# Kernel tuning notes

Hardware: AMD Instinct MI355X
Metric: run time of the kernel (lower is better)

## Reference

```python
import jax, jax.numpy as jnp
import numpy as np

NUM_HEADS = 8
LN_EPS = 1e-3  # keras LayerNormalization default epsilon


def _layer_norm(z, gamma, beta):
    m = jnp.mean(z, axis=-1, keepdims=True)
    v = jnp.mean(jnp.square(z - m), axis=-1, keepdims=True)
    return (z - m) * jax.lax.rsqrt(v + LN_EPS) * gamma + beta


def _swish(z):
    return z * jax.nn.sigmoid(z)


def setup_inputs() -> dict:
    key = jax.random.key(0)
    ks = jax.random.split(key, 9)
    B, T, F, U = 64, 256, 512, 1024
    he = lambda k, s: jax.random.normal(k, s, jnp.float32) * np.sqrt(2.0 / s[0])
    glorot = lambda k, s: jax.random.normal(k, s, jnp.float32) * np.sqrt(2.0 / (s[0] + s[1]))
    return {
        "x": jax.random.normal(ks[0], (B, T, F), jnp.float32),
        "kernel_x": he(ks[1], (F, U)),
        "kernel_h": he(ks[2], (U, U)),
        "W_q": glorot(ks[3], (U, U)),
        "W_k": glorot(ks[4], (U, U)),
        "W_v": glorot(ks[5], (U, U)),
        "W_o": glorot(ks[6], (U, U)),
        "W_f": glorot(ks[7], (U, U)),
        "W_i": glorot(ks[8], (U, U)),
        "ln1_gamma": jnp.ones((U,), jnp.float32),
        "ln1_beta": jnp.zeros((U,), jnp.float32),
        "ln2_gamma": jnp.ones((U,), jnp.float32),
        "ln2_beta": jnp.zeros((U,), jnp.float32),
    }


def reference(x, kernel_x, kernel_h, W_q, W_k, W_v, W_o, W_f, W_i,
              ln1_gamma, ln1_beta, ln2_gamma, ln2_beta):
    B, T, F = x.shape
    U = kernel_x.shape[1]
    H = NUM_HEADS
    D = U // H
    scale = 1.0 / np.sqrt(D)

    def step(carry, x_t):
        h_prev, c_prev = carry  # c_prev = layer-normed longterm from last step
        xx = x_t @ kernel_x + h_prev @ kernel_h           # [B,U]
        f = jax.nn.sigmoid(xx @ W_f)
        i = jax.nn.sigmoid(xx @ W_i)
        cand = jnp.tanh(xx)
        longterm = f * c_prev + i * cand
        shortterm = _swish(longterm + _swish(xx))
        shortterm = _layer_norm(shortterm, ln1_gamma, ln1_beta)
        longterm = _layer_norm(longterm, ln2_gamma, ln2_beta)
        # mini self-attention where the "sequence" axis is the 8 heads
        q = (shortterm @ W_q).reshape(B, H, D)
        k = (shortterm @ W_k).reshape(B, H, D)
        v = (shortterm @ W_v).reshape(B, H, D)
        scores = jnp.einsum("bhd,bgd->bhg", q, k) * scale  # [B,H,H]
        weights = jax.nn.softmax(scores, axis=-1)
        attended = jnp.einsum("bhg,bgd->bhd", weights, v).reshape(B, U)
        out = shortterm + attended @ W_o
        return (out, longterm), out

    init = (jnp.zeros((B, U), x.dtype), jnp.zeros((B, U), x.dtype))
    _, ys = jax.lax.scan(step, init, jnp.swapaxes(x, 0, 1))  # ys: [T,B,U]
    return jnp.swapaxes(ys, 0, 1)  # [B,T,U]
```

## Files before the change

kernel.cpp:

```cpp
#include <hip/hip_runtime.h>

#define NB 64
#define NT 256
#define NF 512
#define NU 1024
#define NWG 256
#define NTHR 256
#define SLICE 65536

typedef float f32x4 __attribute__((ext_vector_type(4)));

__device__ __forceinline__ float sigm(float x) { return 1.f / (1.f + __expf(-x)); }

__device__ __forceinline__ f32x4 ld_cg4(const float* p) {
  f32x4 t;
  asm volatile("global_load_dwordx4 %0, %1, off sc0 sc1" : "=&v"(t) : "v"(p));
  return t;
}
__device__ __forceinline__ float ld_cg1(const float* p) {
  float t;
  asm volatile("global_load_dword %0, %1, off sc0 sc1" : "=&v"(t) : "v"(p));
  return t;
}
__device__ __forceinline__ f32x4 ld_nc4(const float* p) {
  f32x4 t;
  asm volatile("global_load_dwordx4 %0, %1, off" : "=&v"(t) : "v"(p));
  return t;
}
__device__ __forceinline__ void vm_wait() {
  asm volatile("s_waitcnt vmcnt(0)" ::: "memory");
  __builtin_amdgcn_sched_barrier(0);
}

struct KParams {
  const float *x, *g1, *b1, *g2, *b2;
  const float *Wx, *Wh, *Wf, *Wi, *Wq, *Wk, *Wv, *Wo;
  float *out;
  float *xp, *qkvp, *wop, *attb, *sp, *stats;
  float *WhWf, *WhWi, *WxWf, *WxWi;
  int *flags, *grel;
};

__device__ __forceinline__ void grid_barrier(int* flags, int* grel, int epoch,
                                             int wg, int tid, bool dirty) {
  asm volatile("s_waitcnt vmcnt(0) lgkmcnt(0)" ::: "memory");
  __syncthreads();
  if (wg == 0) {
    if (tid > 0) {
      while (__hip_atomic_load(&flags[tid * 16], __ATOMIC_RELAXED, __HIP_MEMORY_SCOPE_AGENT) < epoch)
        __builtin_amdgcn_s_sleep(1);
    }
    __syncthreads();
    if (tid == 0)
      __builtin_amdgcn_fence(__ATOMIC_RELEASE, "agent");
    __syncthreads();
    if (tid < 16)
      __hip_atomic_store(&grel[tid * 16], epoch, __ATOMIC_RELAXED, __HIP_MEMORY_SCOPE_AGENT);
    __syncthreads();
  } else {
    if (tid == 0) {
      if (dirty)
        __builtin_amdgcn_fence(__ATOMIC_RELEASE, "agent");
      __hip_atomic_store(&flags[wg * 16], epoch, __ATOMIC_RELAXED, __HIP_MEMORY_SCOPE_AGENT);
      const int g = wg >> 4;
      while (__hip_atomic_load(&grel[g * 16], __ATOMIC_RELAXED, __HIP_MEMORY_SCOPE_AGENT) < epoch)
        __builtin_amdgcn_s_sleep(1);
    }
    __syncthreads();
  }
}

__device__ __forceinline__ void gemm_tile(
    float* As, float* Wl, const float* smm, const float* smr,
    int mode, const float* A0, size_t a_ld,
    const float* g1, const float* b1, const float* wop,
    float* outw, size_t out_ld,
    const float* __restrict__ W, int n0, int k0, int nchunks,
    float* __restrict__ dst, int tid)
{
  const int cg = tid & 15, rg = tid >> 4;
  const int c0 = cg * 4, r0 = rg * 4;
  float4 acc0 = {0,0,0,0}, acc1 = {0,0,0,0}, acc2 = {0,0,0,0}, acc3 = {0,0,0,0};

  for (int cc = 0; cc < nchunks; ++cc) {
    const int kc = k0 + cc * 64;
    __syncthreads();

    f32x4 wv[4];
#pragma unroll
    for (int it = 0; it < 4; ++it) {
      int idx = tid + it * 256;
      int kk = idx >> 4, cgs = idx & 15;
      wv[it] = ld_nc4(W + (size_t)(kc + kk) * NU + n0 + cgs * 4);
    }

    f32x4 v[4];
    if (mode == 0) {
#pragma unroll
      for (int it = 0; it < 4; ++it) {
        int idx = tid + it * 256;
        int r = idx >> 4, k4 = (idx & 15) << 2;
        v[it] = ld_nc4(A0 + (size_t)r * a_ld + kc + k4);
      }
    } else if (mode == 4) {
#pragma unroll
      for (int it = 0; it < 4; ++it) {
        int idx = tid + it * 256;
        int r = idx >> 4, k4 = (idx & 15) << 2;
        v[it] = ld_cg4(A0 + (size_t)r * a_ld + kc + k4);
      }
    } else if (mode == 3) {
      f32x4 av[4];
#pragma unroll
      for (int it = 0; it < 4; ++it) {
        int idx = tid + it * 256;
        int r = idx >> 4, k4 = (idx & 15) << 2;
        av[it] = ld_cg4(A0 + (size_t)r * NU + kc + k4);
      }
      vm_wait();
#pragma unroll
      for (int it = 0; it < 4; ++it) {
        int idx = tid + it * 256;
        int r = idx >> 4, k4 = (idx & 15) << 2;
        int col = kc + k4;
        float m = smm[r], rs = smr[r];
        f32x4 g  = *(const f32x4*)(g1 + col);
        f32x4 be = *(const f32x4*)(b1 + col);
        v[it] = (av[it] - m) * rs * g + be;
      }
    } else {
      if (A0) {
        f32x4 sv[4], w0v[4], w1v[4];
#pragma unroll
        for (int it = 0; it < 4; ++it) {
          int idx = tid + it * 256;
          int r = idx >> 4, k4 = (idx & 15) << 2;
          int col = kc + k4;
          sv[it]  = ld_cg4(A0 + (size_t)r * NU + col);
          w0v[it] = ld_cg4(wop + 0 * SLICE + (size_t)r * NU + col);
          w1v[it] = ld_cg4(wop + 1 * SLICE + (size_t)r * NU + col);
        }
        vm_wait();
        f32x4 pp[4];
#pragma unroll
        for (int it = 0; it < 4; ++it) {
          int idx = tid + it * 256;
          int r = idx >> 4, k4 = (idx & 15) << 2;
          int col = kc + k4;
          float m = smm[r], rs = smr[r];
          f32x4 g  = *(const f32x4*)(g1 + col);
          f32x4 be = *(const f32x4*)(b1 + col);
          pp[it] = (sv[it] - m) * rs * g + be + w0v[it] + w1v[it];
        }
#pragma unroll
        for (int it = 0; it < 4; ++it) {
          int idx = tid + it * 256;
          int r = idx >> 4, k4 = (idx & 15) << 2;
          int col = kc + k4;
          w0v[it] = ld_cg4(wop + 2 * SLICE + (size_t)r * NU + col);
          w1v[it] = ld_cg4(wop + 3 * SLICE + (size_t)r * NU + col);
        }
        vm_wait();
#pragma unroll
        for (int it = 0; it < 4; ++it) {
          int idx = tid + it * 256;
          int r = idx >> 4, k4 = (idx & 15) << 2;
          v[it] = pp[it] + w0v[it] + w1v[it];
          if (outw) *(f32x4*)(outw + (size_t)r * out_ld + kc + k4) = v[it];
        }
      } else {
#pragma unroll
        for (int it = 0; it < 4; ++it) v[it] = (f32x4){0.f, 0.f, 0.f, 0.f};
      }
    }

    vm_wait();
#pragma unroll
    for (int it = 0; it < 4; ++it) {
      int idx = tid + it * 256;
      int r = idx >> 4, k4 = (idx & 15) << 2;
      *(f32x4*)(&As[r * 68 + k4]) = v[it];
    }
#pragma unroll
    for (int it = 0; it < 4; ++it) {
      int idx = tid + it * 256;
      int kk = idx >> 4, cgs = idx & 15;
      int sw = (((kk >> 2) ^ cgs) & 15) << 2;
      int base = (cgs * 4) * 68 + sw + (kk & 3);
      Wl[base] = wv[it].x; Wl[base + 68] = wv[it].y; Wl[base + 136] = wv[it].z; Wl[base + 204] = wv[it].w;
    }
    __syncthreads();
#pragma unroll
    for (int kk = 0; kk < 64; kk += 4) {
      int sw = ((((kk >> 2) ^ cg) & 15) << 2);
      const float4 w0 = *(const float4*)(&Wl[(c0 + 0) * 68 + sw]);
      const float4 w1 = *(const float4*)(&Wl[(c0 + 1) * 68 + sw]);
      const float4 w2 = *(const float4*)(&Wl[(c0 + 2) * 68 + sw]);
      const float4 w3 = *(const float4*)(&Wl[(c0 + 3) * 68 + sw]);
      const float4 a0 = *(const float4*)(&As[(r0 + 0) * 68 + kk]);
      const float4 a1 = *(const float4*)(&As[(r0 + 1) * 68 + kk]);
      const float4 a2 = *(const float4*)(&As[(r0 + 2) * 68 + kk]);
      const float4 a3 = *(const float4*)(&As[(r0 + 3) * 68 + kk]);
#define DOT4(ac, av) \
      ac.x = fmaf(av.x, w0.x, fmaf(av.y, w0.y, fmaf(av.z, w0.z, fmaf(av.w, w0.w, ac.x)))); \
      ac.y = fmaf(av.x, w1.x, fmaf(av.y, w1.y, fmaf(av.z, w1.z, fmaf(av.w, w1.w, ac.y)))); \
      ac.z = fmaf(av.x, w2.x, fmaf(av.y, w2.y, fmaf(av.z, w2.z, fmaf(av.w, w2.w, ac.z)))); \
      ac.w = fmaf(av.x, w3.x, fmaf(av.y, w3.y, fmaf(av.z, w3.z, fmaf(av.w, w3.w, ac.w))));
      DOT4(acc0, a0) DOT4(acc1, a1) DOT4(acc2, a2) DOT4(acc3, a3)
#undef DOT4
    }
  }
  *(float4*)(dst + (size_t)(r0 + 0) * NU + n0 + c0) = acc0;
  *(float4*)(dst + (size_t)(r0 + 1) * NU + n0 + c0) = acc1;
  *(float4*)(dst + (size_t)(r0 + 2) * NU + n0 + c0) = acc2;
  *(float4*)(dst + (size_t)(r0 + 3) * NU + n0 + c0) = acc3;
}

__device__ __forceinline__ void run_xjob(const KParams& p, float* As, float* Wl,
                                         int t, int j, int tid) {
  const int out = j >> 5, rest = j & 31;
  const int xs = rest >> 4, nt = rest & 15;
  const float* W = (out == 0) ? p.Wx : (out == 1) ? p.WxWf : p.WxWi;
  gemm_tile(As, Wl, nullptr, nullptr, 0, p.x + (size_t)t * NF, (size_t)NT * NF,
            nullptr, nullptr, nullptr, nullptr, 0,
            W, nt * 64, xs * 256, 4,
            p.xp + (size_t)(out * 6 + 4 + xs) * SLICE, tid);
}

__global__ __launch_bounds__(NTHR, 1) void vecaw_main(KParams p) {
  const int wg = blockIdx.x;
  const int tid = threadIdx.x;

  __shared__ __align__(16) float As[64 * 68];
  __shared__ __align__(16) float Wl[64 * 68];
  __shared__ float smm[64], smr[64], red[16], att_s[64];

  int epoch = 0;
  f32x4 c_reg = {0.f, 0.f, 0.f, 0.f};

  for (int r = 0; r < 3; ++r) {
    int j = r * 256 + wg;
    const float *A0, *W; float *dst; int jj;
    if (j < 256)      { jj = j;       A0 = p.Wh; W = p.Wf; dst = p.WhWf; }
    else if (j < 512) { jj = j - 256; A0 = p.Wh; W = p.Wi; dst = p.WhWi; }
    else if (j < 640) { jj = j - 512; A0 = p.Wx; W = p.Wf; dst = p.WxWf; }
    else              { jj = j - 640; A0 = p.Wx; W = p.Wi; dst = p.WxWi; }
    const int rb = jj >> 4, nt = jj & 15;
    gemm_tile(As, Wl, nullptr, nullptr, 0, A0 + (size_t)rb * 64 * NU, NU,
              nullptr, nullptr, nullptr, nullptr, 0,
              W, nt * 64, 0, 16, dst + (size_t)rb * 64 * NU, tid);
    grid_barrier(p.flags, p.grel, ++epoch, wg, tid, true);
  }
  if (wg < 96) run_xjob(p, As, Wl, 0, wg, tid);
  grid_barrier(p.flags, p.grel, ++epoch, wg, tid, wg < 96);

  for (int t = 0; t < NT; ++t) {

    if (wg < 192) {
      const int out = wg >> 6, idx = wg & 63, nt = idx & 15, ks = idx >> 4;
      if (tid < 64 && t > 0) {
        float m = ld_cg1(p.stats + tid);
        float r = ld_cg1(p.stats + 64 + tid);
        vm_wait();
        smm[tid] = m; smr[tid] = r;
      }
      const float* W = (out == 0) ? p.Wh : (out == 1) ? p.WhWf : p.WhWi;
      float* outw = (out == 0 && nt == 0 && t > 0) ? (p.out + (size_t)(t - 1) * NU) : nullptr;
      gemm_tile(As, Wl, smm, smr, 1, (t > 0) ? p.sp : nullptr, NU,
                p.g1, p.b1, p.wop, outw, (size_t)NT * NU,
                W, nt * 64, ks * 256, 4,
                p.xp + (size_t)(out * 6 + ks) * SLICE, tid);
    }
    grid_barrier(p.flags, p.grel, ++epoch, wg, tid, wg < 192);

    if (wg < 64) {
      const int b = wg;
      const size_t off = (size_t)b * NU + tid * 4;
      f32x4 a[18];
#pragma unroll
      for (int s = 0; s < 18; ++s) a[s] = ld_cg4(p.xp + (size_t)s * SLICE + off);
      vm_wait();
      f32x4 xx = a[0] + a[1] + a[2] + a[3] + a[4] + a[5];
      f32x4 fs = a[6] + a[7] + a[8] + a[9] + a[10] + a[11];
      f32x4 is = a[12] + a[13] + a[14] + a[15] + a[16] + a[17];
      f32x4 ltq, spq;
#define P2COMP(C) { \
      float xxv = xx.C; \
      float f = sigm(fs.C), i = sigm(is.C); \
      float ltv = f * c_reg.C + i * tanhf(xxv); \
      float sw = xxv * sigm(xxv); \
      float spin = ltv + sw; \
      ltq.C = ltv; spq.C = spin * sigm(spin); }
      P2COMP(x) P2COMP(y) P2COMP(z) P2COMP(w)
#undef P2COMP
      *(f32x4*)(p.sp + off) = spq;
      float s0 = spq.x + spq.y + spq.z + spq.w;
      float s1 = spq.x*spq.x + spq.y*spq.y + spq.z*spq.z + spq.w*spq.w;
      float s2 = ltq.x + ltq.y + ltq.z + ltq.w;
      float s3 = ltq.x*ltq.x + ltq.y*ltq.y + ltq.z*ltq.z + ltq.w*ltq.w;
#pragma unroll
      for (int m = 1; m < 64; m <<= 1) {
        s0 += __shfl_xor(s0, m, 64); s1 += __shfl_xor(s1, m, 64);
        s2 += __shfl_xor(s2, m, 64); s3 += __shfl_xor(s3, m, 64);
      }
      if ((tid & 63) == 0) {
        int wv = tid >> 6;
        red[wv * 4 + 0] = s0; red[wv * 4 + 1] = s1;
        red[wv * 4 + 2] = s2; red[wv * 4 + 3] = s3;
      }
      __syncthreads();
      {
        float S0 = red[0] + red[4] + red[8]  + red[12];
        float S1 = red[1] + red[5] + red[9]  + red[13];
        float S2 = red[2] + red[6] + red[10] + red[14];
        float S3 = red[3] + red[7] + red[11] + red[15];
        float m1 = S0 * (1.f / 1024.f), v1 = S1 * (1.f / 1024.f) - m1 * m1;
        float m2 = S2 * (1.f / 1024.f), v2 = S3 * (1.f / 1024.f) - m2 * m2;
        float rs2 = rsqrtf(v2 + 1e-3f);
        f32x4 g2v = *(const f32x4*)(p.g2 + tid * 4);
        f32x4 b2v = *(const f32x4*)(p.b2 + tid * 4);
        c_reg = (ltq - m2) * rs2 * g2v + b2v;
        if (tid == 0) {
          p.stats[b]      = m1;
          p.stats[64 + b] = rsqrtf(v1 + 1e-3f);
        }
      }
    }
    grid_barrier(p.flags, p.grel, ++epoch, wg, tid, wg < 64);

    if (wg < 192) {
      if (tid < 64) {
        float m = ld_cg1(p.stats + tid);
        float r = ld_cg1(p.stats + 64 + tid);
        vm_wait();
        smm[tid] = m; smr[tid] = r;
      }
      const int mat = wg >> 6, idx = wg & 63, nt = idx & 15, ks = idx >> 4;
      const float* W = (mat == 0) ? p.Wq : (mat == 1) ? p.Wk : p.Wv;
      gemm_tile(As, Wl, smm, smr, 3, p.sp, NU,
                p.g1, p.b1, nullptr, nullptr, 0,
                W, nt * 64, ks * 256, 4, p.qkvp + (size_t)(mat * 4 + ks) * SLICE, tid);
    }
    grid_barrier(p.flags, p.grel, ++epoch, wg, tid, wg < 192);

    if (wg < 64) {
      const int b = wg;
      f32x4 q0[3], q1[3], q2[3], q3[3];
#pragma unroll
      for (int it = 0; it < 3; ++it) {
        int e4 = (tid + it * 256) * 4;
        int m = e4 >> 10, d = e4 & 1023;
        const float* base = p.qkvp + (size_t)(m * 4) * SLICE + (size_t)b * NU + d;
        q0[it] = ld_cg4(base);
        q1[it] = ld_cg4(base + SLICE);
        q2[it] = ld_cg4(base + 2 * SLICE);
        q3[it] = ld_cg4(base + 3 * SLICE);
      }
      vm_wait();
#pragma unroll
      for (int it = 0; it < 3; ++it) {
        int e4 = (tid + it * 256) * 4;
        f32x4 s = q0[it] + q1[it] + q2[it] + q3[it];
        *(f32x4*)(&As[e4]) = s;
      }
      __syncthreads();
      if (tid < 64) {
        int h = tid >> 3, g = tid & 7;
        float s = 0.f;
#pragma unroll 8
        for (int d = 0; d < 128; ++d) s = fmaf(As[h * 128 + d], As[1024 + g * 128 + d], s);
        att_s[tid] = s * 0.08838834764831845f;
      }
      __syncthreads();
      if (tid < 8) {
        float mx = -1e30f;
#pragma unroll
        for (int g = 0; g < 8; ++g) mx = fmaxf(mx, att_s[tid * 8 + g]);
        float e8[8], sum = 0.f;
#pragma unroll
        for (int g = 0; g < 8; ++g) { e8[g] = __expf(att_s[tid * 8 + g] - mx); sum += e8[g]; }
        float inv = 1.f / sum;
#pragma unroll
        for (int g = 0; g < 8; ++g) att_s[tid * 8 + g] = e8[g] * inv;
      }
      __syncthreads();
      {
        int idx4 = tid * 4;
        int h = idx4 >> 7, d = idx4 & 127;
        f32x4 a = {0.f, 0.f, 0.f, 0.f};
#pragma unroll
        for (int g = 0; g < 8; ++g) {
          float w = att_s[h * 8 + g];
          a += w * (*(const f32x4*)(&As[2048 + g * 128 + d]));
        }
        *(f32x4*)(p.attb + (size_t)b * NU + idx4) = a;
      }
    } else if (wg < 160 && t + 1 < NT) {
      run_xjob(p, As, Wl, t + 1, wg - 64, tid);
    }
    grid_barrier(p.flags, p.grel, ++epoch, wg, tid, wg < 160);

    if (wg < 64) {
      const int nt = wg & 15, ks = wg >> 4;
      gemm_tile(As, Wl, nullptr, nullptr, 4, p.attb, NU,
                nullptr, nullptr, nullptr, nullptr, 0,
                p.Wo, nt * 64, ks * 256, 4, p.wop + (size_t)ks * SLICE, tid);
    }
    grid_barrier(p.flags, p.grel, ++epoch, wg, tid, wg < 64);
  }

  if (wg < 64) {
    const int b = wg;
    const int u4 = tid * 4;
    const size_t off = (size_t)b * NU + u4;
    float m  = ld_cg1(p.stats + b);
    float rs = ld_cg1(p.stats + 64 + b);
    f32x4 s4 = ld_cg4(p.sp + off);
    f32x4 w0 = ld_cg4(p.wop + off);
    f32x4 w1 = ld_cg4(p.wop + SLICE + off);
    f32x4 w2 = ld_cg4(p.wop + 2 * SLICE + off);
    f32x4 w3 = ld_cg4(p.wop + 3 * SLICE + off);
    vm_wait();
    f32x4 g  = *(const f32x4*)(p.g1 + u4);
    f32x4 be = *(const f32x4*)(p.b1 + u4);
    f32x4 o = (s4 - m) * rs * g + be + w0 + w1 + w2 + w3;
    *(f32x4*)(p.out + ((size_t)b * NT + 255) * NU + u4) = o;
  }
}

extern "C" void kernel_launch(void* const* d_in, const int* in_sizes, int n_in,
                              void* d_out, int out_size, void* d_ws, size_t ws_size,
                              hipStream_t stream) {
  (void)in_sizes; (void)n_in; (void)out_size; (void)ws_size;
  const float* x  = (const float*)d_in[0];
  const float* Wx = (const float*)d_in[1];
  const float* Wh = (const float*)d_in[2];
  const float* Wq = (const float*)d_in[3];
  const float* Wk = (const float*)d_in[4];
  const float* Wv = (const float*)d_in[5];
  const float* Wo = (const float*)d_in[6];
  const float* Wf = (const float*)d_in[7];
  const float* Wi = (const float*)d_in[8];
  const float* g1 = (const float*)d_in[9];
  const float* b1 = (const float*)d_in[10];
  const float* g2 = (const float*)d_in[11];
  const float* b2 = (const float*)d_in[12];

  char* pp = (char*)d_ws;
  auto take = [&](size_t bytes) { char* r = pp; pp += (bytes + 255) & ~(size_t)255; return r; };
  int*   flags = (int*)take(256 * 16 * 4);
  int*   grel  = (int*)take(16 * 16 * 4);
  float* stats = (float*)take(256 * 4);
  size_t zbytes = (size_t)(pp - (char*)d_ws);
  float* xp    = (float*)take((size_t)18 * SLICE * 4);
  float* qkvp  = (float*)take((size_t)12 * SLICE * 4);
  float* wop   = (float*)take((size_t)4 * SLICE * 4);
  float* attb  = (float*)take((size_t)SLICE * 4);
  float* sp    = (float*)take((size_t)SLICE * 4);
  float* WhWf  = (float*)take((size_t)16 * SLICE * 4);
  float* WhWi  = (float*)take((size_t)16 * SLICE * 4);
  float* WxWf  = (float*)take((size_t)8 * SLICE * 4);
  float* WxWi  = (float*)take((size_t)8 * SLICE * 4);

  hipMemsetAsync(d_ws, 0, zbytes, stream);

  KParams kp;
  kp.x = x; kp.g1 = g1; kp.b1 = b1; kp.g2 = g2; kp.b2 = b2;
  kp.Wx = Wx; kp.Wh = Wh; kp.Wf = Wf; kp.Wi = Wi;
  kp.Wq = Wq; kp.Wk = Wk; kp.Wv = Wv; kp.Wo = Wo;
  kp.out = (float*)d_out;
  kp.xp = xp; kp.qkvp = qkvp; kp.wop = wop; kp.attb = attb; kp.sp = sp;
  kp.stats = stats;
  kp.WhWf = WhWf; kp.WhWi = WhWi; kp.WxWf = WxWf; kp.WxWi = WxWi;
  kp.flags = flags; kp.grel = grel;

  vecaw_main<<<dim3(NWG), dim3(NTHR), 0, stream>>>(kp);
}
```

Baseline: 21.65 ms.

## Precompute Wo·Wh products and split recurrent GEMM to cut a grid barrier per step

Since h_t = LN1(short) + attended@Wo, the recurrent projections h@Wh, h@WhWf and h@WhWi are split into a LN1(short) term and an attended term. The attended term uses precomputed products Wo·Wh, Wo·WhWf and Wo·WhWi. The LN term is computed alongside attention, and the attended term alongside the Wo output GEMM, so each timestep has one fewer full-grid barrier and the output write moves into the QKV phase. This costs three extra 1024x1024 weight products at startup, more partial-sum buffers (double-buffered sp, stats and x-projections), and different floating-point association of the results.

```diff
diff --git a/kernel.cpp b/kernel.cpp
--- a/kernel.cpp
+++ b/kernel.cpp
@@ -36,8 +36,14 @@
   const float *x, *g1, *b1, *g2, *b2;
   const float *Wx, *Wh, *Wf, *Wi, *Wq, *Wk, *Wv, *Wo;
   float *out;
-  float *xp, *qkvp, *wop, *attb, *sp, *stats;
-  float *WhWf, *WhWi, *WxWf, *WxWi;
+  float *xp;
+  float *xjp;
+  float *qkvp;
+  float *wop;
+  float *attb;
+  float *sp;
+  float *stats;
+  float *WhWf, *WhWi, *WxWf, *WxWi, *WoWh, *WoWhWf, *WoWhWi;
   int *flags, *grel;
 };
 
@@ -73,8 +79,7 @@
 __device__ __forceinline__ void gemm_tile(
     float* As, float* Wl, const float* smm, const float* smr,
     int mode, const float* A0, size_t a_ld,
-    const float* g1, const float* b1, const float* wop,
-    float* outw, size_t out_ld,
+    const float* g1, const float* b1,
     const float* __restrict__ W, int n0, int k0, int nchunks,
     float* __restrict__ dst, int tid)
 {
@@ -109,7 +114,7 @@
         int r = idx >> 4, k4 = (idx & 15) << 2;
         v[it] = ld_cg4(A0 + (size_t)r * a_ld + kc + k4);
       }
-    } else if (mode == 3) {
+    } else {
       f32x4 av[4];
 #pragma unroll
       for (int it = 0; it < 4; ++it) {
@@ -127,50 +132,6 @@
         f32x4 g  = *(const f32x4*)(g1 + col);
         f32x4 be = *(const f32x4*)(b1 + col);
         v[it] = (av[it] - m) * rs * g + be;
-      }
-    } else {
-      if (A0) {
-        f32x4 sv[4], w0v[4], w1v[4];
-#pragma unroll
-        for (int it = 0; it < 4; ++it) {
-          int idx = tid + it * 256;
-          int r = idx >> 4, k4 = (idx & 15) << 2;
-          int col = kc + k4;
-          sv[it]  = ld_cg4(A0 + (size_t)r * NU + col);
-          w0v[it] = ld_cg4(wop + 0 * SLICE + (size_t)r * NU + col);
-          w1v[it] = ld_cg4(wop + 1 * SLICE + (size_t)r * NU + col);
-        }
-        vm_wait();
-        f32x4 pp[4];
-#pragma unroll
-        for (int it = 0; it < 4; ++it) {
-          int idx = tid + it * 256;
-          int r = idx >> 4, k4 = (idx & 15) << 2;
-          int col = kc + k4;
-          float m = smm[r], rs = smr[r];
-          f32x4 g  = *(const f32x4*)(g1 + col);
-          f32x4 be = *(const f32x4*)(b1 + col);
-          pp[it] = (sv[it] - m) * rs * g + be + w0v[it] + w1v[it];
-        }
-#pragma unroll
-        for (int it = 0; it < 4; ++it) {
-          int idx = tid + it * 256;
-          int r = idx >> 4, k4 = (idx & 15) << 2;
-          int col = kc + k4;
-          w0v[it] = ld_cg4(wop + 2 * SLICE + (size_t)r * NU + col);
-          w1v[it] = ld_cg4(wop + 3 * SLICE + (size_t)r * NU + col);
-        }
-        vm_wait();
-#pragma unroll
-        for (int it = 0; it < 4; ++it) {
-          int idx = tid + it * 256;
-          int r = idx >> 4, k4 = (idx & 15) << 2;
-          v[it] = pp[it] + w0v[it] + w1v[it];
-          if (outw) *(f32x4*)(outw + (size_t)r * out_ld + kc + k4) = v[it];
-        }
-      } else {
-#pragma unroll
-        for (int it = 0; it < 4; ++it) v[it] = (f32x4){0.f, 0.f, 0.f, 0.f};
       }
     }
 
@@ -218,13 +179,12 @@
 
 __device__ __forceinline__ void run_xjob(const KParams& p, float* As, float* Wl,
                                          int t, int j, int tid) {
-  const int out = j >> 5, rest = j & 31;
+  const int o = j >> 5, rest = j & 31;
   const int xs = rest >> 4, nt = rest & 15;
-  const float* W = (out == 0) ? p.Wx : (out == 1) ? p.WxWf : p.WxWi;
+  const float* W = (o == 0) ? p.Wx : (o == 1) ? p.WxWf : p.WxWi;
+  float* dst = p.xjp + ((size_t)(t & 1) * 6 + o * 2 + xs) * SLICE;
   gemm_tile(As, Wl, nullptr, nullptr, 0, p.x + (size_t)t * NF, (size_t)NT * NF,
-            nullptr, nullptr, nullptr, nullptr, 0,
-            W, nt * 64, xs * 256, 4,
-            p.xp + (size_t)(out * 6 + 4 + xs) * SLICE, tid);
+            nullptr, nullptr, W, nt * 64, xs * 256, 4, dst, tid);
 }
 
 __global__ __launch_bounds__(NTHR, 1) void vecaw_main(KParams p) {
@@ -247,53 +207,57 @@
     else              { jj = j - 640; A0 = p.Wx; W = p.Wi; dst = p.WxWi; }
     const int rb = jj >> 4, nt = jj & 15;
     gemm_tile(As, Wl, nullptr, nullptr, 0, A0 + (size_t)rb * 64 * NU, NU,
-              nullptr, nullptr, nullptr, nullptr, 0,
-              W, nt * 64, 0, 16, dst + (size_t)rb * 64 * NU, tid);
+              nullptr, nullptr, W, nt * 64, 0, 16, dst + (size_t)rb * 64 * NU, tid);
+    grid_barrier(p.flags, p.grel, ++epoch, wg, tid, true);
+  }
+  for (int r = 0; r < 3; ++r) {
+    int j = r * 256 + wg;
+    const float *W; float *dst; int jj;
+    if (j < 256)      { jj = j;       W = p.Wh;   dst = p.WoWh;   }
+    else if (j < 512) { jj = j - 256; W = p.WhWf; dst = p.WoWhWf; }
+    else              { jj = j - 512; W = p.WhWi; dst = p.WoWhWi; }
+    const int rb = jj >> 4, nt = jj & 15;
+    gemm_tile(As, Wl, nullptr, nullptr, 0, p.Wo + (size_t)rb * 64 * NU, NU,
+              nullptr, nullptr, W, nt * 64, 0, 16, dst + (size_t)rb * 64 * NU, tid);
     grid_barrier(p.flags, p.grel, ++epoch, wg, tid, true);
   }
   if (wg < 96) run_xjob(p, As, Wl, 0, wg, tid);
   grid_barrier(p.flags, p.grel, ++epoch, wg, tid, wg < 96);
 
   for (int t = 0; t < NT; ++t) {
-
-    if (wg < 192) {
-      const int out = wg >> 6, idx = wg & 63, nt = idx & 15, ks = idx >> 4;
-      if (tid < 64 && t > 0) {
-        float m = ld_cg1(p.stats + tid);
-        float r = ld_cg1(p.stats + 64 + tid);
-        vm_wait();
-        smm[tid] = m; smr[tid] = r;
-      }
-      const float* W = (out == 0) ? p.Wh : (out == 1) ? p.WhWf : p.WhWi;
-      float* outw = (out == 0 && nt == 0 && t > 0) ? (p.out + (size_t)(t - 1) * NU) : nullptr;
-      gemm_tile(As, Wl, smm, smr, 1, (t > 0) ? p.sp : nullptr, NU,
-                p.g1, p.b1, p.wop, outw, (size_t)NT * NU,
-                W, nt * 64, ks * 256, 4,
-                p.xp + (size_t)(out * 6 + ks) * SLICE, tid);
-    }
-    grid_barrier(p.flags, p.grel, ++epoch, wg, tid, wg < 192);
+    const int par = t & 1;
 
     if (wg < 64) {
       const int b = wg;
       const size_t off = (size_t)b * NU + tid * 4;
-      f32x4 a[18];
-#pragma unroll
-      for (int s = 0; s < 18; ++s) a[s] = ld_cg4(p.xp + (size_t)s * SLICE + off);
+      f32x4 a0[10], a1[10], a2[10];
+#pragma unroll
+      for (int s = 0; s < 8; ++s) {
+        a0[s] = ld_cg4(p.xp + (size_t)(0 * 8 + s) * SLICE + off);
+        a1[s] = ld_cg4(p.xp + (size_t)(1 * 8 + s) * SLICE + off);
+        a2[s] = ld_cg4(p.xp + (size_t)(2 * 8 + s) * SLICE + off);
+      }
+#pragma unroll
+      for (int s = 0; s < 2; ++s) {
+        a0[8 + s] = ld_cg4(p.xjp + ((size_t)par * 6 + 0 * 2 + s) * SLICE + off);
+        a1[8 + s] = ld_cg4(p.xjp + ((size_t)par * 6 + 1 * 2 + s) * SLICE + off);
+        a2[8 + s] = ld_cg4(p.xjp + ((size_t)par * 6 + 2 * 2 + s) * SLICE + off);
+      }
       vm_wait();
-      f32x4 xx = a[0] + a[1] + a[2] + a[3] + a[4] + a[5];
-      f32x4 fs = a[6] + a[7] + a[8] + a[9] + a[10] + a[11];
-      f32x4 is = a[12] + a[13] + a[14] + a[15] + a[16] + a[17];
+      f32x4 xx = a0[0], fs = a1[0], is = a2[0];
+#pragma unroll
+      for (int s = 1; s < 10; ++s) { xx += a0[s]; fs += a1[s]; is += a2[s]; }
       f32x4 ltq, spq;
-#define P2COMP(C) { \
+#define PACOMP(C) { \
       float xxv = xx.C; \
       float f = sigm(fs.C), i = sigm(is.C); \
       float ltv = f * c_reg.C + i * tanhf(xxv); \
       float sw = xxv * sigm(xxv); \
       float spin = ltv + sw; \
       ltq.C = ltv; spq.C = spin * sigm(spin); }
-      P2COMP(x) P2COMP(y) P2COMP(z) P2COMP(w)
-#undef P2COMP
-      *(f32x4*)(p.sp + off) = spq;
+      PACOMP(x) PACOMP(y) PACOMP(z) PACOMP(w)
+#undef PACOMP
+      *(f32x4*)(p.sp + (size_t)par * SLICE + off) = spq;
       float s0 = spq.x + spq.y + spq.z + spq.w;
       float s1 = spq.x*spq.x + spq.y*spq.y + spq.z*spq.z + spq.w*spq.w;
       float s2 = ltq.x + ltq.y + ltq.z + ltq.w;
@@ -321,25 +285,43 @@
         f32x4 b2v = *(const f32x4*)(p.b2 + tid * 4);
         c_reg = (ltq - m2) * rs2 * g2v + b2v;
         if (tid == 0) {
-          p.stats[b]      = m1;
-          p.stats[64 + b] = rsqrtf(v1 + 1e-3f);
+          p.stats[par * 128 + b]      = m1;
+          p.stats[par * 128 + 64 + b] = rsqrtf(v1 + 1e-3f);
         }
       }
-    }
-    grid_barrier(p.flags, p.grel, ++epoch, wg, tid, wg < 64);
+    } else if (wg < 160 && t + 1 < NT) {
+      run_xjob(p, As, Wl, t + 1, wg - 64, tid);
+    }
+    grid_barrier(p.flags, p.grel, ++epoch, wg, tid, wg < 160);
 
     if (wg < 192) {
       if (tid < 64) {
-        float m = ld_cg1(p.stats + tid);
-        float r = ld_cg1(p.stats + 64 + tid);
+        float m = ld_cg1(p.stats + par * 128 + tid);
+        float r = ld_cg1(p.stats + par * 128 + 64 + tid);
         vm_wait();
         smm[tid] = m; smr[tid] = r;
       }
       const int mat = wg >> 6, idx = wg & 63, nt = idx & 15, ks = idx >> 4;
       const float* W = (mat == 0) ? p.Wq : (mat == 1) ? p.Wk : p.Wv;
-      gemm_tile(As, Wl, smm, smr, 3, p.sp, NU,
-                p.g1, p.b1, nullptr, nullptr, 0,
-                W, nt * 64, ks * 256, 4, p.qkvp + (size_t)(mat * 4 + ks) * SLICE, tid);
+      gemm_tile(As, Wl, smm, smr, 3, p.sp + (size_t)par * SLICE, NU,
+                p.g1, p.b1, W, nt * 64, ks * 256, 4,
+                p.qkvp + (size_t)(mat * 4 + ks) * SLICE, tid);
+    } else if (t > 0) {
+      const int b = wg - 192, pold = (t - 1) & 1;
+      const int u4 = tid * 4;
+      const size_t off = (size_t)b * NU + u4;
+      float m  = ld_cg1(p.stats + pold * 128 + b);
+      float rs = ld_cg1(p.stats + pold * 128 + 64 + b);
+      f32x4 s4 = ld_cg4(p.sp + (size_t)pold * SLICE + off);
+      f32x4 w0 = ld_cg4(p.wop + off);
+      f32x4 w1 = ld_cg4(p.wop + SLICE + off);
+      f32x4 w2 = ld_cg4(p.wop + 2 * SLICE + off);
+      f32x4 w3 = ld_cg4(p.wop + 3 * SLICE + off);
+      vm_wait();
+      f32x4 g  = *(const f32x4*)(p.g1 + u4);
+      f32x4 be = *(const f32x4*)(p.b1 + u4);
+      f32x4 o = (s4 - m) * rs * g + be + w0 + w1 + w2 + w3;
+      *(f32x4*)(p.out + ((size_t)b * NT + (t - 1)) * NU + u4) = o;
     }
     grid_barrier(p.flags, p.grel, ++epoch, wg, tid, wg < 192);
 
@@ -395,27 +377,45 @@
         }
         *(f32x4*)(p.attb + (size_t)b * NU + idx4) = a;
       }
-    } else if (wg < 160 && t + 1 < NT) {
-      run_xjob(p, As, Wl, t + 1, wg - 64, tid);
-    }
-    grid_barrier(p.flags, p.grel, ++epoch, wg, tid, wg < 160);
-
-    if (wg < 64) {
-      const int nt = wg & 15, ks = wg >> 4;
+    } else if (t + 1 < NT) {
+      if (tid < 64) {
+        float m = ld_cg1(p.stats + par * 128 + tid);
+        float r = ld_cg1(p.stats + par * 128 + 64 + tid);
+        vm_wait();
+        smm[tid] = m; smr[tid] = r;
+      }
+      const int j = wg - 64, o = j >> 6, idx = j & 63, nt = idx & 15, ks = idx >> 4;
+      const float* W = (o == 0) ? p.Wh : (o == 1) ? p.WhWf : p.WhWi;
+      gemm_tile(As, Wl, smm, smr, 3, p.sp + (size_t)par * SLICE, NU,
+                p.g1, p.b1, W, nt * 64, ks * 256, 4,
+                p.xp + (size_t)(o * 8 + ks) * SLICE, tid);
+    }
+    grid_barrier(p.flags, p.grel, ++epoch, wg, tid, (wg < 64) || (t + 1 < NT));
+
+    if (wg < 192) {
+      if (t + 1 < NT) {
+        const int o = wg >> 6, idx = wg & 63, nt = idx & 15, ks = idx >> 4;
+        const float* W = (o == 0) ? p.WoWh : (o == 1) ? p.WoWhWf : p.WoWhWi;
+        gemm_tile(As, Wl, nullptr, nullptr, 4, p.attb, NU,
+                  nullptr, nullptr, W, nt * 64, ks * 256, 4,
+                  p.xp + (size_t)(o * 8 + 4 + ks) * SLICE, tid);
+      }
+    } else {
+      const int idx = wg - 192, nt = idx & 15, ks = idx >> 4;
       gemm_tile(As, Wl, nullptr, nullptr, 4, p.attb, NU,
-                nullptr, nullptr, nullptr, nullptr, 0,
-                p.Wo, nt * 64, ks * 256, 4, p.wop + (size_t)ks * SLICE, tid);
-    }
-    grid_barrier(p.flags, p.grel, ++epoch, wg, tid, wg < 64);
-  }
-
-  if (wg < 64) {
-    const int b = wg;
+                nullptr, nullptr, p.Wo, nt * 64, ks * 256, 4,
+                p.wop + (size_t)ks * SLICE, tid);
+    }
+    grid_barrier(p.flags, p.grel, ++epoch, wg, tid, (wg >= 192) || (t + 1 < NT));
+  }
+
+  if (wg >= 192) {
+    const int b = wg - 192;
     const int u4 = tid * 4;
     const size_t off = (size_t)b * NU + u4;
-    float m  = ld_cg1(p.stats + b);
-    float rs = ld_cg1(p.stats + 64 + b);
-    f32x4 s4 = ld_cg4(p.sp + off);
+    float m  = ld_cg1(p.stats + 128 + b);
+    float rs = ld_cg1(p.stats + 128 + 64 + b);
+    f32x4 s4 = ld_cg4(p.sp + SLICE + off);
     f32x4 w0 = ld_cg4(p.wop + off);
     f32x4 w1 = ld_cg4(p.wop + SLICE + off);
     f32x4 w2 = ld_cg4(p.wop + 2 * SLICE + off);
@@ -450,17 +450,21 @@
   auto take = [&](size_t bytes) { char* r = pp; pp += (bytes + 255) & ~(size_t)255; return r; };
   int*   flags = (int*)take(256 * 16 * 4);
   int*   grel  = (int*)take(16 * 16 * 4);
-  float* stats = (float*)take(256 * 4);
+  float* stats = (float*)take(2 * 128 * 4);
+  float* xp    = (float*)take((size_t)24 * SLICE * 4);
   size_t zbytes = (size_t)(pp - (char*)d_ws);
-  float* xp    = (float*)take((size_t)18 * SLICE * 4);
-  float* qkvp  = (float*)take((size_t)12 * SLICE * 4);
-  float* wop   = (float*)take((size_t)4 * SLICE * 4);
-  float* attb  = (float*)take((size_t)SLICE * 4);
-  float* sp    = (float*)take((size_t)SLICE * 4);
-  float* WhWf  = (float*)take((size_t)16 * SLICE * 4);
-  float* WhWi  = (float*)take((size_t)16 * SLICE * 4);
-  float* WxWf  = (float*)take((size_t)8 * SLICE * 4);
-  float* WxWi  = (float*)take((size_t)8 * SLICE * 4);
+  float* xjp    = (float*)take((size_t)12 * SLICE * 4);
+  float* qkvp   = (float*)take((size_t)12 * SLICE * 4);
+  float* wop    = (float*)take((size_t)4 * SLICE * 4);
+  float* attb   = (float*)take((size_t)SLICE * 4);
+  float* sp     = (float*)take((size_t)2 * SLICE * 4);
+  float* WhWf   = (float*)take((size_t)16 * SLICE * 4);
+  float* WhWi   = (float*)take((size_t)16 * SLICE * 4);
+  float* WxWf   = (float*)take((size_t)8 * SLICE * 4);
+  float* WxWi   = (float*)take((size_t)8 * SLICE * 4);
+  float* WoWh   = (float*)take((size_t)16 * SLICE * 4);
+  float* WoWhWf = (float*)take((size_t)16 * SLICE * 4);
+  float* WoWhWi = (float*)take((size_t)16 * SLICE * 4);
 
   hipMemsetAsync(d_ws, 0, zbytes, stream);
 
@@ -469,9 +473,10 @@
   kp.Wx = Wx; kp.Wh = Wh; kp.Wf = Wf; kp.Wi = Wi;
   kp.Wq = Wq; kp.Wk = Wk; kp.Wv = Wv; kp.Wo = Wo;
   kp.out = (float*)d_out;
-  kp.xp = xp; kp.qkvp = qkvp; kp.wop = wop; kp.attb = attb; kp.sp = sp;
-  kp.stats = stats;
+  kp.xp = xp; kp.xjp = xjp; kp.qkvp = qkvp; kp.wop = wop;
+  kp.attb = attb; kp.sp = sp; kp.stats = stats;
   kp.WhWf = WhWf; kp.WhWi = WhWi; kp.WxWf = WxWf; kp.WxWi = WxWi;
+  kp.WoWh = WoWh; kp.WoWhWf = WoWhWf; kp.WoWhWi = WoWhWi;
   kp.flags = flags; kp.grel = grel;
 
   vecaw_main<<<dim3(NWG), dim3(NTHR), 0, stream>>>(kp);
```

Measured after the change: 20.80 ms. -3.9%, faster.
